# Kernel tuning notes

Measured on AMD Instinct MI355X. Metric: run time of the kernel, lower is better.

Reference implementation:

```python
import jax, jax.numpy as jnp
import numpy as np


def setup_inputs() -> dict:
    key = jax.random.key(0)
    k1, k2, k3 = jax.random.split(key, 3)
    B, N, F, K, C = 16, 128, 64, 128, 3
    scalar_features = jax.random.normal(k1, (B, N, F), dtype=jnp.float32)
    distances = jax.random.normal(k2, (B, N, N, C), dtype=jnp.float32)
    w_sv = jax.random.normal(k3, (2 * F, K), dtype=jnp.float32) * (1.0 / np.sqrt(2 * F))
    b_sv = jnp.zeros((K,), dtype=jnp.float32)
    return {"scalar_features": scalar_features, "distances": distances,
            "w_sv": w_sv, "b_sv": b_sv}


def reference(scalar_features, distances, w_sv, b_sv):
    # Original: pair[b,i,j] = concat(x[b,i], x[b,j]) @ w_sv + b_sv
    # Split the matmul instead of materializing the concat: x_i @ Wa + x_j @ Wb.
    F = scalar_features.shape[-1]
    wa, wb = w_sv[:F], w_sv[F:]
    pa = jnp.einsum('bif,fk->bik', scalar_features, wa)   # [B,N,K]
    pb = jnp.einsum('bjf,fk->bjk', scalar_features, wb)   # [B,N,K]
    pair = pa[:, :, None, :] + pb[:, None, :, :] + b_sv   # [B,N,N,K]
    # Broadcast over coor_dims and multiply with distances; activation is linear.
    out = pair[:, :, :, None, :] * distances[..., None]   # [B,N,N,3,K]
    return out
```

## Files before the change

kernel.cpp:

```cpp
#include <hip/hip_runtime.h>


#define BN   2048
#define FF   64
#define KK   128

__global__ __launch_bounds__(128) void proj_kernel(
    const float* __restrict__ S,
    const float* __restrict__ W,
    const float* __restrict__ bias,
    float* __restrict__ pa,
    float* __restrict__ pb)
{
    __shared__ float s[FF];
    const int r = blockIdx.x;
    const int k = threadIdx.x;
    if (k < FF) s[k] = S[r * FF + k];
    __syncthreads();

    float acc_a = bias[k];
    float acc_b = 0.0f;
#pragma unroll
    for (int f = 0; f < FF; ++f) {
        const float sv = s[f];
        acc_a = fmaf(sv, W[f * KK + k], acc_a);
        acc_b = fmaf(sv, W[(f + FF) * KK + k], acc_b);
    }
    pa[r * KK + k] = acc_a;
    pb[r * KK + k] = acc_b;
}

__global__ __launch_bounds__(256) void expand_kernel(
    const float* __restrict__ dist,
    const float* __restrict__ pa,
    const float* __restrict__ pb,
    float* __restrict__ out)
{
    const int bi = blockIdx.x;
    const int b  = bi >> 7;
    const int tid = threadIdx.x;

    __shared__ float4 paB[KK / 4];
    if (tid < KK / 4) paB[tid] = ((const float4*)pa)[bi * (KK / 4) + tid];
    __syncthreads();

    const float*  dist_bi = dist + (size_t)bi * 128 * 3;
    const float4* pb_b    = (const float4*)pb + (size_t)b * 128 * (KK / 4);
    float4*       out_bi  = (float4*)out + (size_t)bi * 12288;

#pragma unroll 4
    for (int f = tid; f < 12288; f += 256) {
        const int j  = f / 96;
        const int r  = f - j * 96;
        const int c  = r >> 5;
        const int kq = r & 31;

        const float4 p = paB[kq];
        const float4 q = pb_b[j * 32 + kq];
        const float  d = dist_bi[j * 3 + c];

        float4 o;
        o.x = (p.x + q.x) * d;
        o.y = (p.y + q.y) * d;
        o.z = (p.z + q.z) * d;
        o.w = (p.w + q.w) * d;
        out_bi[f] = o;
    }
}

extern "C" void kernel_launch(void* const* d_in, const int* in_sizes, int n_in,
                              void* d_out, int out_size, void* d_ws, size_t ws_size,
                              hipStream_t stream) {
    const float* S    = (const float*)d_in[0];
    const float* dist = (const float*)d_in[1];
    const float* W    = (const float*)d_in[2];
    const float* bias = (const float*)d_in[3];
    float* out = (float*)d_out;

    float* pa = (float*)d_ws;
    float* pb = pa + (size_t)BN * KK;

    proj_kernel<<<BN, 128, 0, stream>>>(S, W, bias, pa, pb);
    expand_kernel<<<BN, 256, 0, stream>>>(dist, pa, pb, out);
}
```

Baseline: 428.9 us.

## Restructure expand kernel with 384-thread blocks, hoisted indices and nontemporal stores

The expand kernel now runs 384 threads per block, so each thread keeps a fixed (c, kq) lane and its pa vector in registers across 32 iterations. This removes the per-iteration integer division and index math. The row's distances are staged in shared memory, and the output is written with nontemporal stores to avoid polluting the cache on the large write stream. The cost is higher register pressure, a larger block size and a different pb access stride.

```diff
diff --git a/kernel.cpp b/kernel.cpp
--- a/kernel.cpp
+++ b/kernel.cpp
@@ -4,6 +4,8 @@
 #define BN   2048
 #define FF   64
 #define KK   128
+
+typedef float f4 __attribute__((ext_vector_type(4)));
 
 __global__ __launch_bounds__(128) void proj_kernel(
     const float* __restrict__ S,
@@ -30,7 +32,7 @@
     pb[r * KK + k] = acc_b;
 }
 
-__global__ __launch_bounds__(256) void expand_kernel(
+__global__ __launch_bounds__(384) void expand_kernel(
     const float* __restrict__ dist,
     const float* __restrict__ pa,
     const float* __restrict__ pb,
@@ -38,33 +40,33 @@
 {
     const int bi = blockIdx.x;
     const int b  = bi >> 7;
-    const int tid = threadIdx.x;
+    const int t  = threadIdx.x;
 
-    __shared__ float4 paB[KK / 4];
-    if (tid < KK / 4) paB[tid] = ((const float4*)pa)[bi * (KK / 4) + tid];
+    const int jt = t / 96;
+    const int rr = t - jt * 96;
+    const int c  = rr >> 5;
+    const int kq = rr & 31;
+
+    __shared__ float dls[384];
+    dls[t] = dist[(size_t)bi * 384 + t];
+
+    const f4 p = ((const f4*)pa)[bi * (KK / 4) + kq];
     __syncthreads();
 
-    const float*  dist_bi = dist + (size_t)bi * 128 * 3;
-    const float4* pb_b    = (const float4*)pb + (size_t)b * 128 * (KK / 4);
-    float4*       out_bi  = (float4*)out + (size_t)bi * 12288;
+    const f4* __restrict__ pb_p = (const f4*)pb + ((size_t)b * 128) * (KK / 4) + jt * (KK / 4) + kq;
+    const float* __restrict__ dp = &dls[jt * 3 + c];
+    f4* __restrict__ out_p = (f4*)out + (size_t)bi * 12288 + t;
 
-#pragma unroll 4
-    for (int f = tid; f < 12288; f += 256) {
-        const int j  = f / 96;
-        const int r  = f - j * 96;
-        const int c  = r >> 5;
-        const int kq = r & 31;
-
-        const float4 p = paB[kq];
-        const float4 q = pb_b[j * 32 + kq];
-        const float  d = dist_bi[j * 3 + c];
-
-        float4 o;
+#pragma unroll 8
+    for (int it = 0; it < 32; ++it) {
+        const f4    q = pb_p[it * 128];
+        const float d = dp[it * 12];
+        f4 o;
         o.x = (p.x + q.x) * d;
         o.y = (p.y + q.y) * d;
         o.z = (p.z + q.z) * d;
         o.w = (p.w + q.w) * d;
-        out_bi[f] = o;
+        __builtin_nontemporal_store(o, out_p + it * 384);
     }
 }
 
@@ -81,5 +83,5 @@
     float* pb = pa + (size_t)BN * KK;
 
     proj_kernel<<<BN, 128, 0, stream>>>(S, W, bias, pa, pb);
-    expand_kernel<<<BN, 256, 0, stream>>>(dist, pa, pb, out);
+    expand_kernel<<<BN, 384, 0, stream>>>(dist, pa, pb, out);
 }
```

Measured after the change: 412.5 us. -3.8%, faster.

## Restructure expand kernel so each thread reuses one pb vector across i rows

Applied to the files above, without the earlier changes.

Each thread now owns a fixed (j, c, kq) slot and loops over 16 batches, handling two i rows per iteration. That lets one pb load serve two outputs and drops the per-element divide and the shared-memory staging of pa. Outputs are written with nontemporal stores to avoid polluting cache on this write-bound kernel, and the block size goes to 384. Consecutive iterations write far-apart output regions, which may hurt DRAM write locality.

```diff
diff --git a/kernel.cpp b/kernel.cpp
--- a/kernel.cpp
+++ b/kernel.cpp
@@ -4,6 +4,8 @@
 #define BN   2048
 #define FF   64
 #define KK   128
+
+typedef float f4 __attribute__((ext_vector_type(4)));
 
 __global__ __launch_bounds__(128) void proj_kernel(
     const float* __restrict__ S,
@@ -30,41 +32,48 @@
     pb[r * KK + k] = acc_b;
 }
 
-__global__ __launch_bounds__(256) void expand_kernel(
+__global__ __launch_bounds__(384) void expand_kernel(
     const float* __restrict__ dist,
     const float* __restrict__ pa,
     const float* __restrict__ pb,
     float* __restrict__ out)
 {
-    const int bi = blockIdx.x;
-    const int b  = bi >> 7;
-    const int tid = threadIdx.x;
+    const int g = blockIdx.x;
+    const int t = threadIdx.x;
 
-    __shared__ float4 paB[KK / 4];
-    if (tid < KK / 4) paB[tid] = ((const float4*)pa)[bi * (KK / 4) + tid];
-    __syncthreads();
+    const int q  = g >> 5;
+    const int f  = (g & 31) * 384 + t;
+    const int j  = f / 96;
+    const int r  = f - j * 96;
+    const int c  = r >> 5;
+    const int kq = r & 31;
 
-    const float*  dist_bi = dist + (size_t)bi * 128 * 3;
-    const float4* pb_b    = (const float4*)pb + (size_t)b * 128 * (KK / 4);
-    float4*       out_bi  = (float4*)out + (size_t)bi * 12288;
+    const f4*    __restrict__ pa_p   = (const f4*)pa + (size_t)q * 32 + kq;
+    const f4*    __restrict__ pb_p   = (const f4*)pb + (size_t)j * 32 + kq;
+    const float* __restrict__ dist_p = dist + (size_t)q * 384 + (size_t)j * 3 + c;
+    f4*          __restrict__ out_p  = (f4*)out + (size_t)g * 384 + t;
 
 #pragma unroll 4
-    for (int f = tid; f < 12288; f += 256) {
-        const int j  = f / 96;
-        const int r  = f - j * 96;
-        const int c  = r >> 5;
-        const int kq = r & 31;
+    for (int it2 = 0; it2 < 16; ++it2) {
+        const f4    p0 = pa_p[0];
+        const f4    p1 = pa_p[2048];
+        const f4    qq = pb_p[0];
+        const float d0 = dist_p[0];
+        const float d1 = dist_p[24576];
 
-        const float4 p = paB[kq];
-        const float4 q = pb_b[j * 32 + kq];
-        const float  d = dist_bi[j * 3 + c];
+        f4 o0, o1;
+        o0.x = (p0.x + qq.x) * d0;  o1.x = (p1.x + qq.x) * d1;
+        o0.y = (p0.y + qq.y) * d0;  o1.y = (p1.y + qq.y) * d1;
+        o0.z = (p0.z + qq.z) * d0;  o1.z = (p1.z + qq.z) * d1;
+        o0.w = (p0.w + qq.w) * d0;  o1.w = (p1.w + qq.w) * d1;
 
-        float4 o;
-        o.x = (p.x + q.x) * d;
-        o.y = (p.y + q.y) * d;
-        o.z = (p.z + q.z) * d;
-        o.w = (p.w + q.w) * d;
-        out_bi[f] = o;
+        __builtin_nontemporal_store(o0, out_p);
+        __builtin_nontemporal_store(o1, out_p + 786432);
+
+        pa_p   += 4096;
+        pb_p   += 4096;
+        dist_p += 49152;
+        out_p  += 1572864;
     }
 }
 
@@ -81,5 +90,5 @@
     float* pb = pa + (size_t)BN * KK;
 
     proj_kernel<<<BN, 128, 0, stream>>>(S, W, bias, pa, pb);
-    expand_kernel<<<BN, 256, 0, stream>>>(dist, pa, pb, out);
+    expand_kernel<<<BN, 384, 0, stream>>>(dist, pa, pb, out);
 }
```

Result: no change. 420.8 us (-1.9%).

## Restructure expand kernel as grid-stride over rows with fixed per-thread offsets

Applied to the files above, without the earlier changes.

The expand kernel now launches 256 blocks of 384 threads. Each thread keeps fixed (j, c, kq) indices and steps through rows with stride 8, so the per-iteration index division is removed and the shared-memory staging of pa and its barrier disappear. The pa, pb and dist values are read straight from global memory through the cache instead. The change cuts integer and address arithmetic, but it shrinks the grid to 256 blocks, which may lower occupancy and memory-level parallelism for this store-bound kernel.

```diff
diff --git a/kernel.cpp b/kernel.cpp
--- a/kernel.cpp
+++ b/kernel.cpp
@@ -4,6 +4,8 @@
 #define BN   2048
 #define FF   64
 #define KK   128
+
+typedef float f4 __attribute__((ext_vector_type(4)));
 
 __global__ __launch_bounds__(128) void proj_kernel(
     const float* __restrict__ S,
@@ -30,41 +32,45 @@
     pb[r * KK + k] = acc_b;
 }
 
-__global__ __launch_bounds__(256) void expand_kernel(
+__global__ __launch_bounds__(384) void expand_kernel(
     const float* __restrict__ dist,
     const float* __restrict__ pa,
     const float* __restrict__ pb,
     float* __restrict__ out)
 {
-    const int bi = blockIdx.x;
-    const int b  = bi >> 7;
-    const int tid = threadIdx.x;
+    const int gid = blockIdx.x * 384 + threadIdx.x;
 
-    __shared__ float4 paB[KK / 4];
-    if (tid < KK / 4) paB[tid] = ((const float4*)pa)[bi * (KK / 4) + tid];
-    __syncthreads();
+    int row = gid / 12288;
+    const int f  = gid - row * 12288;
+    const int j  = f / 96;
+    const int r  = f - j * 96;
+    const int c  = r >> 5;
+    const int kq = r & 31;
+    const int pboff = j * 32 + kq;
 
-    const float*  dist_bi = dist + (size_t)bi * 128 * 3;
-    const float4* pb_b    = (const float4*)pb + (size_t)b * 128 * (KK / 4);
-    float4*       out_bi  = (float4*)out + (size_t)bi * 12288;
+    const f4*    __restrict__ pa_p   = (const f4*)pa + (size_t)row * 32 + kq;
+    const f4*    __restrict__ pb_b   = (const f4*)pb;
+    const float* __restrict__ dist_p = dist + (size_t)row * 384 + j * 3 + c;
+    f4*          __restrict__ out_p  = (f4*)out + (size_t)gid;
 
-#pragma unroll 4
-    for (int f = tid; f < 12288; f += 256) {
-        const int j  = f / 96;
-        const int r  = f - j * 96;
-        const int c  = r >> 5;
-        const int kq = r & 31;
+#pragma unroll 8
+    for (int it = 0; it < 256; ++it) {
+        const f4    p = pa_p[0];
+        const int   b = row >> 7;
+        const f4    q = pb_b[b * 4096 + pboff];
+        const float d = dist_p[0];
 
-        const float4 p = paB[kq];
-        const float4 q = pb_b[j * 32 + kq];
-        const float  d = dist_bi[j * 3 + c];
-
-        float4 o;
+        f4 o;
         o.x = (p.x + q.x) * d;
         o.y = (p.y + q.y) * d;
         o.z = (p.z + q.z) * d;
         o.w = (p.w + q.w) * d;
-        out_bi[f] = o;
+        out_p[0] = o;
+
+        row    += 8;
+        pa_p   += 256;
+        dist_p += 3072;
+        out_p  += 98304;
     }
 }
 
@@ -81,5 +87,5 @@
     float* pb = pa + (size_t)BN * KK;
 
     proj_kernel<<<BN, 128, 0, stream>>>(S, W, bias, pa, pb);
-    expand_kernel<<<BN, 256, 0, stream>>>(dist, pa, pb, out);
+    expand_kernel<<<256, 384, 0, stream>>>(dist, pa, pb, out);
 }
```

New measurement: 461.5 us. +7.6%, slower.
